# Kernel optimization log

Hardware: AMD Instinct MI355X
Metric: run time of the kernel (lower is better)

## Reference

```python
import jax, jax.numpy as jnp
import numpy as np

N = 50000      # query points (after grid downsampling)
S = 100000     # source points
KN = 32        # neighbors per query
KP = 3         # kernel points per axis -> K = 27
IN = 64
OUT = 64
RADIUS = 0.1
KP_EXTENT = 2.0 * RADIUS / (KP - 1) / (3.0 ** 0.5)
NEG_SLOPE = 0.01  # torch nn.LeakyReLU default


def grid_kernel_points():
    # getKernelPoints: regular 3x3x3 grid in [-radius, radius]^3 -> [27, 3]
    lin = np.linspace(-RADIUS, RADIUS, KP, dtype=np.float32)
    g = np.stack(np.meshgrid(lin, lin, lin, indexing='ij'), axis=-1).reshape(-1, 3)
    return jnp.asarray(g)


def setup_inputs() -> dict:
    key = jax.random.key(0)
    k1, k2, k3, k4, k5, k6 = jax.random.split(key, 6)
    q_pts = jax.random.uniform(k1, (N, 3), dtype=jnp.float32) * 2.0
    s_pts = jax.random.uniform(k2, (S, 3), dtype=jnp.float32) * 2.0
    neighb_inds = jax.random.randint(k3, (N, KN), 0, S, dtype=jnp.int64)
    x = jax.random.normal(k4, (S, IN), dtype=jnp.float32)
    # preactivation Linear(in_fdim -> out_fdim)
    W_pre = jax.random.normal(k5, (IN, OUT), dtype=jnp.float32) * (1.0 / np.sqrt(IN))
    b_pre = jnp.zeros((OUT,), dtype=jnp.float32)
    # KPConv weights [K, conf_in_fdim, out_fdim]; conf_in_fdim = out_fdim (preactivate)
    kp_weights = jax.random.normal(k6, (KP ** 3, OUT, OUT), dtype=jnp.float32) * (1.0 / np.sqrt(KN * OUT))
    kernel_points = grid_kernel_points()
    return {"q_pts": q_pts, "s_pts": s_pts, "neighb_inds": neighb_inds, "x": x,
            "W_pre": W_pre, "b_pre": b_pre, "kp_weights": kp_weights,
            "kernel_points": kernel_points}


def reference(q_pts, s_pts, neighb_inds, x, W_pre, b_pre, kp_weights, kernel_points):
    # --- preactivation: Linear + LeakyReLU (preactivate=True, layernorm=False) ---
    feats = jax.nn.leaky_relu(x @ W_pre + b_pre, negative_slope=NEG_SLOPE)  # [S, OUT]

    # --- KPConv.forward ---
    # append shadow point far away with zero features
    s_pad = jnp.concatenate([s_pts, jnp.full((1, 3), 1e6, s_pts.dtype)], axis=0)      # [S+1, 3]
    f_pad = jnp.concatenate([feats, jnp.zeros((1, feats.shape[-1]), feats.dtype)], 0)  # [S+1, OUT]
    inds = neighb_inds % s_pad.shape[0]                                               # -1 -> shadow index S

    neighbors = s_pad[inds] - q_pts[:, None, :]            # [N, KN, 3]
    neighb_x = f_pad[inds]                                 # [N, KN, OUT]

    diff = neighbors[:, :, None, :] - kernel_points        # [N, KN, K, 3]
    sq_dist = jnp.sum(diff * diff, axis=-1)                # [N, KN, K]
    all_weights = jnp.clip(1.0 - jnp.sqrt(sq_dist) / KP_EXTENT, 0.0)  # linear KP correlation

    # fx[n,o] = sum_{k,l,i} w[n,k,l] * neighb_x[n,k,i] * kp_weights[l,i,o]
    fx = jnp.einsum('nkl,nki,lio->no', all_weights, neighb_x, kp_weights)  # [N, OUT]
    return fx
```

## Files before the change

kernel.cpp:

```cpp
#include <hip/hip_runtime.h>
#include <stdint.h>

#define N_Q   50000
#define N_S   100000
#define KNB   32
#define NKP   27
#define CH    64
#define KP_EXT 0.057735026918962584f
#define BBOX  0.158f
#define NEG_SLOPE 0.01f

__global__ __launch_bounds__(256) void kpconv_kernel(
    const float* __restrict__ q_pts,
    const float* __restrict__ s_pts,
    const int*   __restrict__ inds,
    const float* __restrict__ x,
    const float* __restrict__ W_pre,
    const float* __restrict__ b_pre,
    const float* __restrict__ kp_w,
    const float* __restrict__ kpts,
    float* __restrict__ out)
{
    const int lane = threadIdx.x & 63;
    const int n = (int)((blockIdx.x * (unsigned)blockDim.x + threadIdx.x) >> 6);
    if (n >= N_Q) return;

    const bool i64 = (inds[1] == 0) & (inds[3] == 0) & (inds[5] == 0) & (inds[7] == 0);

    const float qx = q_pts[n * 3 + 0];
    const float qy = q_pts[n * 3 + 1];
    const float qz = q_pts[n * 3 + 2];

    const float e2 = KP_EXT * KP_EXT;

    int   idx = 0;
    float rx = 0.f, ry = 0.f, rz = 0.f;
    bool  hit = false;

    if (lane < KNB) {
        long p = (long)n * KNB + lane;
        long off = i64 ? (2 * p) : p;
        int v = inds[off];
        int m = N_S + 1;
        idx = v % m; if (idx < 0) idx += m;
        if (idx < N_S) {
            rx = s_pts[idx * 3 + 0] - qx;
            ry = s_pts[idx * 3 + 1] - qy;
            rz = s_pts[idx * 3 + 2] - qz;
            if (fabsf(rx) <= BBOX && fabsf(ry) <= BBOX && fabsf(rz) <= BBOX) {
                #pragma unroll 1
                for (int l = 0; l < NKP; ++l) {
                    float dx = rx - kpts[l * 3 + 0];
                    float dy = ry - kpts[l * 3 + 1];
                    float dz = rz - kpts[l * 3 + 2];
                    if (dx * dx + dy * dy + dz * dz < e2) { hit = true; break; }
                }
            }
        }
    }

    unsigned long long mask = __ballot(hit);

    float acc = 0.f;

    while (mask) {
        int src = __ffsll((long long)mask) - 1;
        mask &= mask - 1;

        int   s_idx = __shfl(idx, src, 64);
        float rxs   = __shfl(rx, src, 64);
        float rys   = __shfl(ry, src, 64);
        float rzs   = __shfl(rz, src, 64);

        float xr = x[(long)s_idx * CH + lane];
        float f  = b_pre[lane];
        #pragma unroll
        for (int i = 0; i < CH; ++i) {
            float xi = __shfl(xr, i, 64);
            f = fmaf(xi, W_pre[i * CH + lane], f);
        }
        f = (f >= 0.f) ? f : NEG_SLOPE * f;

        #pragma unroll 1
        for (int l = 0; l < NKP; ++l) {
            float dx = rxs - kpts[l * 3 + 0];
            float dy = rys - kpts[l * 3 + 1];
            float dz = rzs - kpts[l * 3 + 2];
            float d2 = dx * dx + dy * dy + dz * dz;
            if (d2 < e2) {
                float w = 1.f - sqrtf(d2) / KP_EXT;
                const float* Wl = kp_w + (long)l * CH * CH;
                float partial = 0.f;
                #pragma unroll
                for (int i = 0; i < CH; ++i) {
                    float fi = __shfl(f, i, 64);
                    partial = fmaf(fi, Wl[i * CH + lane], partial);
                }
                acc = fmaf(w, partial, acc);
            }
        }
    }

    out[(long)n * CH + lane] = acc;
}

extern "C" void kernel_launch(void* const* d_in, const int* in_sizes, int n_in,
                              void* d_out, int out_size, void* d_ws, size_t ws_size,
                              hipStream_t stream)
{
    const float* q_pts = (const float*)d_in[0];
    const float* s_pts = (const float*)d_in[1];
    const int*   inds  = (const int*)  d_in[2];
    const float* x     = (const float*)d_in[3];
    const float* W_pre = (const float*)d_in[4];
    const float* b_pre = (const float*)d_in[5];
    const float* kp_w  = (const float*)d_in[6];
    const float* kpts  = (const float*)d_in[7];
    float* out = (float*)d_out;

    int blocks = (N_Q + 3) / 4;
    kpconv_kernel<<<blocks, 256, 0, stream>>>(q_pts, s_pts, inds, x,
                                              W_pre, b_pre, kp_w, kpts, out);
}
```

Baseline: 175.6 us.

## Process two queries per wave in a persistent grid with LDS weights and prefetch

Each wave now handles two queries at once, with all 64 lanes testing neighbours (32 per query), where before only half the lanes did useful filtering. A fixed grid of 1024 blocks loops over jobs persistently and prefetches the next job's indices and query coordinates. The preactivation weights, bias and kernel points are staged in LDS once per block. The cost is 16KB of LDS per block and a fixed grid size, and the two halves' hit loops still run one after the other.

After: 153.5 us. 12.6% less time.

```diff
diff --git a/kernel.cpp b/kernel.cpp
--- a/kernel.cpp
+++ b/kernel.cpp
@@ -9,6 +9,7 @@
 #define KP_EXT 0.057735026918962584f
 #define BBOX  0.158f
 #define NEG_SLOPE 0.01f
+#define NJOB  (N_Q / 2)
 
 __global__ __launch_bounds__(256) void kpconv_kernel(
     const float* __restrict__ q_pts,
@@ -21,87 +22,117 @@
     const float* __restrict__ kpts,
     float* __restrict__ out)
 {
+    __shared__ float sW[CH * CH];
+    __shared__ float sB[CH];
+    __shared__ float sKP[NKP * 3];
+
+    for (int i = threadIdx.x; i < CH * CH; i += 256) sW[i] = W_pre[i];
+    if (threadIdx.x < CH)      sB[threadIdx.x]  = b_pre[threadIdx.x];
+    if (threadIdx.x < NKP * 3) sKP[threadIdx.x] = kpts[threadIdx.x];
+    __syncthreads();
+
     const int lane = threadIdx.x & 63;
-    const int n = (int)((blockIdx.x * (unsigned)blockDim.x + threadIdx.x) >> 6);
-    if (n >= N_Q) return;
+    const int gw   = blockIdx.x * (blockDim.x >> 6) + (threadIdx.x >> 6);
+    const int nw   = gridDim.x * (blockDim.x >> 6);
 
     const bool i64 = (inds[1] == 0) & (inds[3] == 0) & (inds[5] == 0) & (inds[7] == 0);
-
-    const float qx = q_pts[n * 3 + 0];
-    const float qy = q_pts[n * 3 + 1];
-    const float qz = q_pts[n * 3 + 2];
-
     const float e2 = KP_EXT * KP_EXT;
 
-    int   idx = 0;
-    float rx = 0.f, ry = 0.f, rz = 0.f;
-    bool  hit = false;
+    int j = gw;
+    int   v_pf = 0;
+    float qx_pf = 0.f, qy_pf = 0.f, qz_pf = 0.f;
+    if (j < NJOB) {
+        long fp = (long)j * 64 + lane;
+        v_pf = inds[i64 ? 2 * fp : fp];
+        long qb = ((long)2 * j + (lane >> 5)) * 3;
+        qx_pf = q_pts[qb + 0];
+        qy_pf = q_pts[qb + 1];
+        qz_pf = q_pts[qb + 2];
+    }
 
-    if (lane < KNB) {
-        long p = (long)n * KNB + lane;
-        long off = i64 ? (2 * p) : p;
-        int v = inds[off];
-        int m = N_S + 1;
-        idx = v % m; if (idx < 0) idx += m;
+    while (j < NJOB) {
+        const int   v  = v_pf;
+        const float qx = qx_pf, qy = qy_pf, qz = qz_pf;
+
+        const int jn = j + nw;
+        if (jn < NJOB) {
+            long fp = (long)jn * 64 + lane;
+            v_pf = inds[i64 ? 2 * fp : fp];
+            long qb = ((long)2 * jn + (lane >> 5)) * 3;
+            qx_pf = q_pts[qb + 0];
+            qy_pf = q_pts[qb + 1];
+            qz_pf = q_pts[qb + 2];
+        }
+
+        const int m_ = N_S + 1;
+        int idx = v % m_; if (idx < 0) idx += m_;
+        float rx = 0.f, ry = 0.f, rz = 0.f;
+        bool hit = false;
         if (idx < N_S) {
-            rx = s_pts[idx * 3 + 0] - qx;
-            ry = s_pts[idx * 3 + 1] - qy;
-            rz = s_pts[idx * 3 + 2] - qz;
+            float sx = s_pts[idx * 3 + 0];
+            float sy = s_pts[idx * 3 + 1];
+            float sz = s_pts[idx * 3 + 2];
+            rx = sx - qx; ry = sy - qy; rz = sz - qz;
             if (fabsf(rx) <= BBOX && fabsf(ry) <= BBOX && fabsf(rz) <= BBOX) {
                 #pragma unroll 1
                 for (int l = 0; l < NKP; ++l) {
-                    float dx = rx - kpts[l * 3 + 0];
-                    float dy = ry - kpts[l * 3 + 1];
-                    float dz = rz - kpts[l * 3 + 2];
+                    float dx = rx - sKP[l * 3 + 0];
+                    float dy = ry - sKP[l * 3 + 1];
+                    float dz = rz - sKP[l * 3 + 2];
                     if (dx * dx + dy * dy + dz * dz < e2) { hit = true; break; }
                 }
             }
         }
-    }
 
-    unsigned long long mask = __ballot(hit);
-
-    float acc = 0.f;
-
-    while (mask) {
-        int src = __ffsll((long long)mask) - 1;
-        mask &= mask - 1;
-
-        int   s_idx = __shfl(idx, src, 64);
-        float rxs   = __shfl(rx, src, 64);
-        float rys   = __shfl(ry, src, 64);
-        float rzs   = __shfl(rz, src, 64);
-
-        float xr = x[(long)s_idx * CH + lane];
-        float f  = b_pre[lane];
-        #pragma unroll
-        for (int i = 0; i < CH; ++i) {
-            float xi = __shfl(xr, i, 64);
-            f = fmaf(xi, W_pre[i * CH + lane], f);
-        }
-        f = (f >= 0.f) ? f : NEG_SLOPE * f;
+        const unsigned long long mask = __ballot(hit);
 
         #pragma unroll 1
-        for (int l = 0; l < NKP; ++l) {
-            float dx = rxs - kpts[l * 3 + 0];
-            float dy = rys - kpts[l * 3 + 1];
-            float dz = rzs - kpts[l * 3 + 2];
-            float d2 = dx * dx + dy * dy + dz * dz;
-            if (d2 < e2) {
-                float w = 1.f - sqrtf(d2) / KP_EXT;
-                const float* Wl = kp_w + (long)l * CH * CH;
-                float partial = 0.f;
+        for (int h = 0; h < 2; ++h) {
+            unsigned long long mh = h ? (mask >> 32)
+                                      : (mask & 0xFFFFFFFFull);
+            float acc = 0.f;
+            while (mh) {
+                int src = (__ffsll((long long)mh) - 1) + (h << 5);
+                mh &= mh - 1;
+
+                int   s_idx = __shfl(idx, src, 64);
+                float rxs   = __shfl(rx, src, 64);
+                float rys   = __shfl(ry, src, 64);
+                float rzs   = __shfl(rz, src, 64);
+
+                float xr = x[(long)s_idx * CH + lane];
+                float f  = sB[lane];
                 #pragma unroll
                 for (int i = 0; i < CH; ++i) {
-                    float fi = __shfl(f, i, 64);
-                    partial = fmaf(fi, Wl[i * CH + lane], partial);
+                    float xi = __shfl(xr, i, 64);
+                    f = fmaf(xi, sW[i * CH + lane], f);
                 }
-                acc = fmaf(w, partial, acc);
+                f = (f >= 0.f) ? f : NEG_SLOPE * f;
+
+                #pragma unroll 1
+                for (int l = 0; l < NKP; ++l) {
+                    float dx = rxs - sKP[l * 3 + 0];
+                    float dy = rys - sKP[l * 3 + 1];
+                    float dz = rzs - sKP[l * 3 + 2];
+                    float d2 = dx * dx + dy * dy + dz * dz;
+                    if (d2 < e2) {
+                        float w = 1.f - sqrtf(d2) / KP_EXT;
+                        const float* Wl = kp_w + (long)l * CH * CH;
+                        float partial = 0.f;
+                        #pragma unroll
+                        for (int i = 0; i < CH; ++i) {
+                            float fi = __shfl(f, i, 64);
+                            partial = fmaf(fi, Wl[i * CH + lane], partial);
+                        }
+                        acc = fmaf(w, partial, acc);
+                    }
+                }
             }
+            out[((long)2 * j + h) * CH + lane] = acc;
         }
+
+        j = jn;
     }
-
-    out[(long)n * CH + lane] = acc;
 }
 
 extern "C" void kernel_launch(void* const* d_in, const int* in_sizes, int n_in,
@@ -118,7 +149,6 @@
     const float* kpts  = (const float*)d_in[7];
     float* out = (float*)d_out;
 
-    int blocks = (N_Q + 3) / 4;
-    kpconv_kernel<<<blocks, 256, 0, stream>>>(q_pts, s_pts, inds, x,
-                                              W_pre, b_pre, kp_w, kpts, out);
+    kpconv_kernel<<<1024, 256, 0, stream>>>(q_pts, s_pts, inds, x,
+                                            W_pre, b_pre, kp_w, kpts, out);
 }
```

## Compact hit neighbor pairs into a global list and process with persistent warps

Applied to the files above, without the earlier changes.

Splits the single kernel into three: zero the output, scan all query-neighbor pairs with a bounding-box test and compact the hits into a workspace list via wave-aggregated atomics, then have a fixed grid of waves walk that list. Each wave computes the preactivation and kernel-point matmuls for one pair and atomically adds into the output. The aim is to stop waves from idling on queries with no hits and to balance the sparse work across the GPU. In exchange it adds two extra launches, a full output memset, and float atomics on the output, which make the summation order nondeterministic. It also drops hits silently if the workspace capacity is exceeded.

Result: slower. 228.3 us (+30.0%).

```diff
diff --git a/kernel.cpp b/kernel.cpp
--- a/kernel.cpp
+++ b/kernel.cpp
@@ -9,8 +9,62 @@
 #define KP_EXT 0.057735026918962584f
 #define BBOX  0.158f
 #define NEG_SLOPE 0.01f
+#define NPAIR (N_Q * KNB)
 
-__global__ __launch_bounds__(256) void kpconv_kernel(
+__global__ __launch_bounds__(256) void init_kernel(float* __restrict__ out,
+                                                   unsigned* __restrict__ counter)
+{
+    int tid = blockIdx.x * 256 + threadIdx.x;
+    if (tid == 0) *counter = 0u;
+    float4* o4 = reinterpret_cast<float4*>(out);
+    const int n4 = (N_Q * CH) / 4;
+    for (int i = tid; i < n4; i += gridDim.x * 256)
+        o4[i] = make_float4(0.f, 0.f, 0.f, 0.f);
+}
+
+__global__ __launch_bounds__(256) void scan_kernel(
+    const float* __restrict__ q_pts,
+    const float* __restrict__ s_pts,
+    const int*   __restrict__ inds,
+    unsigned* __restrict__ counter,
+    unsigned* __restrict__ list,
+    unsigned capacity)
+{
+    const int p = blockIdx.x * 256 + threadIdx.x;
+    const int lane = threadIdx.x & 63;
+
+    const bool i64 = (inds[1] == 0) & (inds[3] == 0) & (inds[5] == 0) & (inds[7] == 0);
+
+    bool hit = false;
+    if (p < NPAIR) {
+        int v = i64 ? reinterpret_cast<const int2*>(inds)[p].x : inds[p];
+        const int m = N_S + 1;
+        int idx = v % m; if (idx < 0) idx += m;
+        if (idx < N_S) {
+            const int n = p >> 5;
+            float rx = s_pts[idx * 3 + 0] - q_pts[n * 3 + 0];
+            float ry = s_pts[idx * 3 + 1] - q_pts[n * 3 + 1];
+            float rz = s_pts[idx * 3 + 2] - q_pts[n * 3 + 2];
+            hit = (fabsf(rx) <= BBOX) & (fabsf(ry) <= BBOX) & (fabsf(rz) <= BBOX);
+        }
+    }
+
+    unsigned long long mask = __ballot(hit);
+    if (mask) {
+        const int leader = __ffsll((long long)mask) - 1;
+        unsigned base = 0u;
+        if (lane == leader)
+            base = atomicAdd(counter, (unsigned)__popcll(mask));
+        base = __shfl(base, leader, 64);
+        if (hit) {
+            unsigned long long lower = mask & ((1ull << lane) - 1ull);
+            unsigned slot = base + (unsigned)__popcll(lower);
+            if (slot < capacity) list[slot] = (unsigned)p;
+        }
+    }
+}
+
+__global__ __launch_bounds__(256) void accum_kernel(
     const float* __restrict__ q_pts,
     const float* __restrict__ s_pts,
     const int*   __restrict__ inds,
@@ -19,60 +73,43 @@
     const float* __restrict__ b_pre,
     const float* __restrict__ kp_w,
     const float* __restrict__ kpts,
+    const unsigned* __restrict__ counter,
+    const unsigned* __restrict__ list,
+    unsigned capacity,
     float* __restrict__ out)
 {
+    unsigned cnt = *counter;
+    if (cnt > capacity) cnt = capacity;
+
     const int lane = threadIdx.x & 63;
-    const int n = (int)((blockIdx.x * (unsigned)blockDim.x + threadIdx.x) >> 6);
-    if (n >= N_Q) return;
+    const int gw = blockIdx.x * (blockDim.x >> 6) + (threadIdx.x >> 6);
+    const int nw = gridDim.x * (blockDim.x >> 6);
 
     const bool i64 = (inds[1] == 0) & (inds[3] == 0) & (inds[5] == 0) & (inds[7] == 0);
-
-    const float qx = q_pts[n * 3 + 0];
-    const float qy = q_pts[n * 3 + 1];
-    const float qz = q_pts[n * 3 + 2];
-
     const float e2 = KP_EXT * KP_EXT;
 
-    int   idx = 0;
-    float rx = 0.f, ry = 0.f, rz = 0.f;
-    bool  hit = false;
+    for (unsigned h = gw; h < cnt; h += nw) {
+        const unsigned p = list[h];
+        const int n = (int)(p >> 5);
+        int v = i64 ? reinterpret_cast<const int2*>(inds)[p].x : inds[(int)p];
+        const int m = N_S + 1;
+        int idx = v % m; if (idx < 0) idx += m;
 
-    if (lane < KNB) {
-        long p = (long)n * KNB + lane;
-        long off = i64 ? (2 * p) : p;
-        int v = inds[off];
-        int m = N_S + 1;
-        idx = v % m; if (idx < 0) idx += m;
-        if (idx < N_S) {
-            rx = s_pts[idx * 3 + 0] - qx;
-            ry = s_pts[idx * 3 + 1] - qy;
-            rz = s_pts[idx * 3 + 2] - qz;
-            if (fabsf(rx) <= BBOX && fabsf(ry) <= BBOX && fabsf(rz) <= BBOX) {
-                #pragma unroll 1
-                for (int l = 0; l < NKP; ++l) {
-                    float dx = rx - kpts[l * 3 + 0];
-                    float dy = ry - kpts[l * 3 + 1];
-                    float dz = rz - kpts[l * 3 + 2];
-                    if (dx * dx + dy * dy + dz * dz < e2) { hit = true; break; }
-                }
-            }
+        const float rx = s_pts[idx * 3 + 0] - q_pts[n * 3 + 0];
+        const float ry = s_pts[idx * 3 + 1] - q_pts[n * 3 + 1];
+        const float rz = s_pts[idx * 3 + 2] - q_pts[n * 3 + 2];
+
+        unsigned active = 0u;
+        #pragma unroll 1
+        for (int l = 0; l < NKP; ++l) {
+            float dx = rx - kpts[l * 3 + 0];
+            float dy = ry - kpts[l * 3 + 1];
+            float dz = rz - kpts[l * 3 + 2];
+            if (dx * dx + dy * dy + dz * dz < e2) active |= (1u << l);
         }
-    }
+        if (active == 0u) continue;
 
-    unsigned long long mask = __ballot(hit);
-
-    float acc = 0.f;
-
-    while (mask) {
-        int src = __ffsll((long long)mask) - 1;
-        mask &= mask - 1;
-
-        int   s_idx = __shfl(idx, src, 64);
-        float rxs   = __shfl(rx, src, 64);
-        float rys   = __shfl(ry, src, 64);
-        float rzs   = __shfl(rz, src, 64);
-
-        float xr = x[(long)s_idx * CH + lane];
+        float xr = x[(long)idx * CH + lane];
         float f  = b_pre[lane];
         #pragma unroll
         for (int i = 0; i < CH; ++i) {
@@ -81,27 +118,27 @@
         }
         f = (f >= 0.f) ? f : NEG_SLOPE * f;
 
-        #pragma unroll 1
-        for (int l = 0; l < NKP; ++l) {
-            float dx = rxs - kpts[l * 3 + 0];
-            float dy = rys - kpts[l * 3 + 1];
-            float dz = rzs - kpts[l * 3 + 2];
+        float acc = 0.f;
+        unsigned am = active;
+        while (am) {
+            int l = __ffs(am) - 1;
+            am &= am - 1;
+            float dx = rx - kpts[l * 3 + 0];
+            float dy = ry - kpts[l * 3 + 1];
+            float dz = rz - kpts[l * 3 + 2];
             float d2 = dx * dx + dy * dy + dz * dz;
-            if (d2 < e2) {
-                float w = 1.f - sqrtf(d2) / KP_EXT;
-                const float* Wl = kp_w + (long)l * CH * CH;
-                float partial = 0.f;
-                #pragma unroll
-                for (int i = 0; i < CH; ++i) {
-                    float fi = __shfl(f, i, 64);
-                    partial = fmaf(fi, Wl[i * CH + lane], partial);
-                }
-                acc = fmaf(w, partial, acc);
+            float w = 1.f - sqrtf(d2) / KP_EXT;
+            const float* Wl = kp_w + (long)l * CH * CH;
+            float partial = 0.f;
+            #pragma unroll
+            for (int i = 0; i < CH; ++i) {
+                float fi = __shfl(f, i, 64);
+                partial = fmaf(fi, Wl[i * CH + lane], partial);
             }
+            acc = fmaf(w, partial, acc);
         }
+        atomicAdd(&out[(long)n * CH + lane], acc);
     }
-
-    out[(long)n * CH + lane] = acc;
 }
 
 extern "C" void kernel_launch(void* const* d_in, const int* in_sizes, int n_in,
@@ -118,7 +155,17 @@
     const float* kpts  = (const float*)d_in[7];
     float* out = (float*)d_out;
 
-    int blocks = (N_Q + 3) / 4;
-    kpconv_kernel<<<blocks, 256, 0, stream>>>(q_pts, s_pts, inds, x,
-                                              W_pre, b_pre, kp_w, kpts, out);
+    unsigned* counter = (unsigned*)d_ws;
+    unsigned* list    = (unsigned*)((char*)d_ws + 128);
+    size_t cap = (ws_size > 128) ? (ws_size - 128) / 4 : 0;
+    if (cap > 2000000) cap = 2000000;
+    unsigned capacity = (unsigned)cap;
+
+    init_kernel<<<2048, 256, 0, stream>>>(out, counter);
+
+    scan_kernel<<<NPAIR / 256, 256, 0, stream>>>(q_pts, s_pts, inds,
+                                                 counter, list, capacity);
+
+    accum_kernel<<<256, 256, 0, stream>>>(q_pts, s_pts, inds, x, W_pre, b_pre,
+                                          kp_w, kpts, counter, list, capacity, out);
 }
```

## Process two queries per wavefront and stage weights and features in LDS

Applied to the files above, without the earlier changes.

Each 64-lane wavefront now handles two query points, one neighbor per lane, so no lanes sit idle during the neighbor-gather and hit-test phase. The grid shrinks to 6250 blocks. The preactivation weight matrix, bias and kernel points are copied into shared memory once per block. Per-neighbor features are broadcast through an LDS row instead of 64 cross-lane shuffles, which adds block-level staging and a per-block load of the 16KB weight matrix.

Result: faster. 160.9 us (-8.4%).

```diff
diff --git a/kernel.cpp b/kernel.cpp
--- a/kernel.cpp
+++ b/kernel.cpp
@@ -21,87 +21,95 @@
     const float* __restrict__ kpts,
     float* __restrict__ out)
 {
+    __shared__ float sW[CH * CH];
+    __shared__ float sB[CH];
+    __shared__ float sKP[NKP * 3];
+    __shared__ float lf[4][CH];
+
+    for (int i = threadIdx.x; i < CH * CH; i += 256) sW[i] = W_pre[i];
+    if (threadIdx.x < CH)      sB[threadIdx.x]  = b_pre[threadIdx.x];
+    if (threadIdx.x < NKP * 3) sKP[threadIdx.x] = kpts[threadIdx.x];
+    __syncthreads();
+
     const int lane = threadIdx.x & 63;
-    const int n = (int)((blockIdx.x * (unsigned)blockDim.x + threadIdx.x) >> 6);
-    if (n >= N_Q) return;
+    const int wid  = threadIdx.x >> 6;
+    const int job  = blockIdx.x * 4 + wid;
 
     const bool i64 = (inds[1] == 0) & (inds[3] == 0) & (inds[5] == 0) & (inds[7] == 0);
-
-    const float qx = q_pts[n * 3 + 0];
-    const float qy = q_pts[n * 3 + 1];
-    const float qz = q_pts[n * 3 + 2];
-
     const float e2 = KP_EXT * KP_EXT;
 
-    int   idx = 0;
+    const long fp = (long)job * 64 + lane;
+    const int  v  = i64 ? reinterpret_cast<const int2*>(inds)[fp].x : inds[fp];
+
+    const int  q  = job * 2 + (lane >> 5);
+    const float qx = q_pts[q * 3 + 0];
+    const float qy = q_pts[q * 3 + 1];
+    const float qz = q_pts[q * 3 + 2];
+
+    const int m_ = N_S + 1;
+    int idx = v % m_; if (idx < 0) idx += m_;
+
     float rx = 0.f, ry = 0.f, rz = 0.f;
-    bool  hit = false;
-
-    if (lane < KNB) {
-        long p = (long)n * KNB + lane;
-        long off = i64 ? (2 * p) : p;
-        int v = inds[off];
-        int m = N_S + 1;
-        idx = v % m; if (idx < 0) idx += m;
-        if (idx < N_S) {
-            rx = s_pts[idx * 3 + 0] - qx;
-            ry = s_pts[idx * 3 + 1] - qy;
-            rz = s_pts[idx * 3 + 2] - qz;
-            if (fabsf(rx) <= BBOX && fabsf(ry) <= BBOX && fabsf(rz) <= BBOX) {
-                #pragma unroll 1
-                for (int l = 0; l < NKP; ++l) {
-                    float dx = rx - kpts[l * 3 + 0];
-                    float dy = ry - kpts[l * 3 + 1];
-                    float dz = rz - kpts[l * 3 + 2];
-                    if (dx * dx + dy * dy + dz * dz < e2) { hit = true; break; }
-                }
+    bool hit = false;
+    if (idx < N_S) {
+        rx = s_pts[idx * 3 + 0] - qx;
+        ry = s_pts[idx * 3 + 1] - qy;
+        rz = s_pts[idx * 3 + 2] - qz;
+        if (fabsf(rx) <= BBOX && fabsf(ry) <= BBOX && fabsf(rz) <= BBOX) {
+            #pragma unroll 1
+            for (int l = 0; l < NKP; ++l) {
+                float dx = rx - sKP[l * 3 + 0];
+                float dy = ry - sKP[l * 3 + 1];
+                float dz = rz - sKP[l * 3 + 2];
+                if (dx * dx + dy * dy + dz * dz < e2) { hit = true; break; }
             }
         }
     }
 
     unsigned long long mask = __ballot(hit);
 
-    float acc = 0.f;
+    float acc0 = 0.f, acc1 = 0.f;
 
     while (mask) {
-        int src = __ffsll((long long)mask) - 1;
+        const int src = __ffsll((long long)mask) - 1;
         mask &= mask - 1;
 
-        int   s_idx = __shfl(idx, src, 64);
-        float rxs   = __shfl(rx, src, 64);
-        float rys   = __shfl(ry, src, 64);
-        float rzs   = __shfl(rz, src, 64);
+        const int   sidx = __shfl(idx, src, 64);
+        const float rxs  = __shfl(rx, src, 64);
+        const float rys  = __shfl(ry, src, 64);
+        const float rzs  = __shfl(rz, src, 64);
 
-        float xr = x[(long)s_idx * CH + lane];
-        float f  = b_pre[lane];
+        lf[wid][lane] = x[(long)sidx * CH + lane];
+
+        float t = sB[lane];
         #pragma unroll
-        for (int i = 0; i < CH; ++i) {
-            float xi = __shfl(xr, i, 64);
-            f = fmaf(xi, W_pre[i * CH + lane], f);
-        }
-        f = (f >= 0.f) ? f : NEG_SLOPE * f;
+        for (int i = 0; i < CH; ++i)
+            t = fmaf(lf[wid][i], sW[i * CH + lane], t);
+        float f = (t >= 0.f) ? t : NEG_SLOPE * t;
+
+        lf[wid][lane] = f;
 
         #pragma unroll 1
         for (int l = 0; l < NKP; ++l) {
-            float dx = rxs - kpts[l * 3 + 0];
-            float dy = rys - kpts[l * 3 + 1];
-            float dz = rzs - kpts[l * 3 + 2];
+            float dx = rxs - sKP[l * 3 + 0];
+            float dy = rys - sKP[l * 3 + 1];
+            float dz = rzs - sKP[l * 3 + 2];
             float d2 = dx * dx + dy * dy + dz * dz;
             if (d2 < e2) {
                 float w = 1.f - sqrtf(d2) / KP_EXT;
-                const float* Wl = kp_w + (long)l * CH * CH;
+                const float* Wl = kp_w + (unsigned)(l * CH * CH);
                 float partial = 0.f;
                 #pragma unroll
-                for (int i = 0; i < CH; ++i) {
-                    float fi = __shfl(f, i, 64);
-                    partial = fmaf(fi, Wl[i * CH + lane], partial);
-                }
-                acc = fmaf(w, partial, acc);
+                for (int i = 0; i < CH; ++i)
+                    partial = fmaf(lf[wid][i], Wl[i * CH + lane], partial);
+                if (src < 32) acc0 = fmaf(w, partial, acc0);
+                else          acc1 = fmaf(w, partial, acc1);
             }
         }
     }
 
-    out[(long)n * CH + lane] = acc;
+    out[((long)job * 2 + 0) * CH + lane] = acc0;
+    out[((long)job * 2 + 1) * CH + lane] = acc1;
 }
 
 extern "C" void kernel_launch(void* const* d_in, const int* in_sizes, int n_in,
@@ -118,7 +126,6 @@
     const float* kpts  = (const float*)d_in[7];
     float* out = (float*)d_out;
 
-    int blocks = (N_Q + 3) / 4;
-    kpconv_kernel<<<blocks, 256, 0, stream>>>(q_pts, s_pts, inds, x,
-                                              W_pre, b_pre, kp_w, kpts, out);
+    kpconv_kernel<<<6250, 256, 0, stream>>>(q_pts, s_pts, inds, x,
+                                            W_pre, b_pre, kp_w, kpts, out);
 }
```
